# Optimization experiments

Measured on AMD Instinct MI355X. Metric: run time of the kernel, lower is better.

## Reference

```python
import jax, jax.numpy as jnp
import numpy as np

N, E, G = 50000, 400000, 256   # nodes, edges, graphs
DIN, DH = 513, 128             # int(256*4/2+1), dim_h
BN_EPS = 1e-5

def _lin_init(k, fin, fout):
    k1, k2 = jax.random.split(k)
    s = 1.0 / np.sqrt(fin)
    w = jax.random.uniform(k1, (fin, fout), jnp.float32, -s, s)
    b = jax.random.uniform(k2, (fout,), jnp.float32, -s, s)
    return w, b

def setup_inputs():
    ks = list(jax.random.split(jax.random.key(0), 20))
    inp = {
        'x': jax.random.normal(ks[0], (N, DIN), jnp.float32),
        'edge_index': jax.random.randint(ks[1], (2, E), 0, N),
        'batch': jnp.sort(jax.random.randint(ks[2], (N,), 0, G)),
    }
    i = 3
    for c in (1, 2, 3):
        fin = DIN if c == 1 else DH
        w1, b1 = _lin_init(ks[i], fin, DH); i += 1
        w2, b2 = _lin_init(ks[i], DH, DH); i += 1
        inp['conv%d_w1' % c], inp['conv%d_b1' % c] = w1, b1
        inp['conv%d_bn_g' % c] = jnp.ones((DH,), jnp.float32)
        inp['conv%d_bn_b' % c] = jnp.zeros((DH,), jnp.float32)
        inp['conv%d_bn_m' % c] = 0.1 * jax.random.normal(ks[i], (DH,), jnp.float32); i += 1
        inp['conv%d_bn_v' % c] = jax.random.uniform(ks[i], (DH,), jnp.float32, 0.5, 1.5); i += 1
        inp['conv%d_w2' % c], inp['conv%d_b2' % c] = w2, b2
    inp['lin1_w'], inp['lin1_b'] = _lin_init(ks[i], 3 * DH, 3 * DH); i += 1
    inp['lin2_w'], inp['lin2_b'] = _lin_init(ks[i], 3 * DH, 3)
    return inp

def _gin_conv(x, src, dst, w1, b1, g, bb, m, v, w2, b2):
    # GINConv, eps=0: MLP((1+eps)*x + sum_{j->i} x_j)
    agg = jax.ops.segment_sum(x[src], dst, num_segments=x.shape[0])
    h = (x + agg) @ w1 + b1
    h = (h - m) * jax.lax.rsqrt(v + BN_EPS) * g + bb   # BatchNorm1d (eval, running stats)
    h = jax.nn.relu(h)
    return jax.nn.relu(h @ w2 + b2)

def _mean_pool(h, batch, num_graphs):
    s = jax.ops.segment_sum(h, batch, num_segments=num_graphs)
    cnt = jax.ops.segment_sum(jnp.ones((h.shape[0],), h.dtype), batch, num_segments=num_graphs)
    return s / jnp.maximum(cnt, 1.0)[:, None]

def reference(x, edge_index, batch, conv1_w1, conv1_b1, conv1_bn_g, conv1_bn_b, conv1_bn_m, conv1_bn_v, conv1_w2, conv1_b2, conv2_w1, conv2_b1, conv2_bn_g, conv2_bn_b, conv2_bn_m, conv2_bn_v, conv2_w2, conv2_b2, conv3_w1, conv3_b1, conv3_bn_g, conv3_bn_b, conv3_bn_m, conv3_bn_v, conv3_w2, conv3_b2, lin1_w, lin1_b, lin2_w, lin2_b):
    src, dst = edge_index[0], edge_index[1]
    h1 = _gin_conv(x, src, dst, conv1_w1, conv1_b1, conv1_bn_g, conv1_bn_b, conv1_bn_m, conv1_bn_v, conv1_w2, conv1_b2)
    h2 = _gin_conv(h1, src, dst, conv2_w1, conv2_b1, conv2_bn_g, conv2_bn_b, conv2_bn_m, conv2_bn_v, conv2_w2, conv2_b2)
    h3 = _gin_conv(h2, src, dst, conv3_w1, conv3_b1, conv3_bn_g, conv3_bn_b, conv3_bn_m, conv3_bn_v, conv3_w2, conv3_b2)
    h = jnp.concatenate([_mean_pool(h1, batch, G), _mean_pool(h2, batch, G), _mean_pool(h3, batch, G)], axis=1)
    h = jax.nn.relu(h @ lin1_w + lin1_b)   # dropout p=0.5 is identity in eval mode
    return h @ lin2_w + lin2_b
```

## Files before the change

### kernel.cpp

```cpp
#include <hip/hip_runtime.h>

#define NN 50000
#define NE 400000
#define NG 256
#define BN_EPS 1e-5f
#define SCAN_E 8
#define SCAN_CHUNK 2048
#define SCAN_NB 25

typedef __attribute__((ext_vector_type(4))) float f32x4;
typedef __bf16 bf16x8 __attribute__((ext_vector_type(8)));
typedef __bf16 bf16x4 __attribute__((ext_vector_type(4)));

__device__ __forceinline__ void mfma_bf16(f32x4& d, bf16x8 a, bf16x8 b) {
  asm volatile("v_mfma_f32_16x16x32_bf16 %0, %1, %2, %0" : "+v"(d) : "v"(a), "v"(b));
}

__global__ __launch_bounds__(256)
void wprep(const float* __restrict__ W, __bf16* __restrict__ wh,
           __bf16* __restrict__ wl, int K, int Kpad) {
  int idx = blockIdx.x * 256 + threadIdx.x;
  if (idx >= 128 * Kpad) return;
  int n = idx & 127, k = idx >> 7;
  float v = (k < K) ? W[(long)k * 128 + n] : 0.f;
  __bf16 h = (__bf16)v;
  wh[(long)n * Kpad + k] = h;
  wl[(long)n * Kpad + k] = (__bf16)(v - (float)h);
}

template<bool BIAS, bool RELU, bool OUT_SPLIT, bool A_FP32>
__global__ __launch_bounds__(512)
void gemm_bsp(const float* __restrict__ Af,
              const __bf16* __restrict__ Ah, const __bf16* __restrict__ Al,
              const __bf16* __restrict__ Wh, const __bf16* __restrict__ Wl,
              const float* __restrict__ bias, float* __restrict__ Cf,
              __bf16* __restrict__ Ch, __bf16* __restrict__ Cl,
              int M, int Kact, int Kpad) {
  __shared__ __align__(16) __bf16 ah[64 * 40];
  __shared__ __align__(16) __bf16 al[64 * 40];
  __shared__ __align__(16) __bf16 bh[128 * 40];
  __shared__ __align__(16) __bf16 bl[128 * 40];
  const int t = threadIdx.x;
  const int row0 = blockIdx.x * 64;
  const int wave = t >> 6, lane = t & 63;
  const int wr = wave >> 2, wc = wave & 3;
  const int lr = lane & 15, kg = lane >> 4;

  const int b_r = (t >> 2) & 127, b_ko = t & 3;
  const __bf16* bh_src = Wh + (long)b_r * Kpad + b_ko * 8;
  const __bf16* bl_src = Wl + (long)b_r * Kpad + b_ko * 8;
  __bf16* bh_dst = bh + b_r * 40 + b_ko * 8;
  __bf16* bl_dst = bl + b_r * 40 + b_ko * 8;

  f32x4 acc[2][2] = {};
  bf16x8 zero8;
#pragma unroll
  for (int j = 0; j < 8; ++j) zero8[j] = (__bf16)0.f;

  const int a_pl = t >> 8, a_r8 = (t >> 2) & 63, a_ko = t & 3;
  const __bf16* a_src = (a_pl ? Al : Ah) + (long)(row0 + a_r8) * Kpad + a_ko * 8;
  __bf16* a_dst = (a_pl ? al : ah) + a_r8 * 40 + a_ko * 8;
  const bool a_ok8 = (row0 + a_r8) < M;
  const int a_rf = t >> 3, a_kq = t & 7;
  const bool a_okf = (row0 + a_rf) < M;
  const float* af_src = Af + (long)(row0 + a_rf) * Kact + a_kq * 4;
  __bf16* ahf_dst = ah + a_rf * 40 + a_kq * 4;
  __bf16* alf_dst = al + a_rf * 40 + a_kq * 4;

  bf16x8 av;
  float fa[4];
  if (A_FP32) {
#pragma unroll
    for (int j = 0; j < 4; ++j) {
      int k = a_kq * 4 + j;
      fa[j] = (a_okf && k < Kact) ? af_src[j] : 0.f;
    }
  } else {
    av = a_ok8 ? *(const bf16x8*)a_src : zero8;
  }
  bf16x8 bv0 = *(const bf16x8*)bh_src;
  bf16x8 bv1 = *(const bf16x8*)bl_src;

  for (int k0 = 0; k0 < Kpad; k0 += 32) {
    __syncthreads();
    if (A_FP32) {
      bf16x4 hv, lv;
#pragma unroll
      for (int j = 0; j < 4; ++j) {
        __bf16 h = (__bf16)fa[j];
        hv[j] = h; lv[j] = (__bf16)(fa[j] - (float)h);
      }
      *(bf16x4*)ahf_dst = hv;
      *(bf16x4*)alf_dst = lv;
    } else {
      *(bf16x8*)a_dst = av;
    }
    *(bf16x8*)bh_dst = bv0;
    *(bf16x8*)bl_dst = bv1;
    __syncthreads();
    int k1 = k0 + 32;
    if (k1 < Kpad) {
      if (A_FP32) {
#pragma unroll
        for (int j = 0; j < 4; ++j) {
          int k = k1 + a_kq * 4 + j;
          fa[j] = (a_okf && k < Kact) ? af_src[k1 + j] : 0.f;
        }
      } else {
        av = a_ok8 ? *(const bf16x8*)(a_src + k1) : zero8;
      }
      bv0 = *(const bf16x8*)(bh_src + k1);
      bv1 = *(const bf16x8*)(bl_src + k1);
    }
    bf16x8 fah[2], fal[2], fbh[2], fbl[2];
#pragma unroll
    for (int mi = 0; mi < 2; ++mi) {
      int r = wr * 32 + mi * 16 + lr;
      fah[mi] = *(const bf16x8*)&ah[r * 40 + kg * 8];
      fal[mi] = *(const bf16x8*)&al[r * 40 + kg * 8];
    }
#pragma unroll
    for (int ni = 0; ni < 2; ++ni) {
      int c = wc * 32 + ni * 16 + lr;
      fbh[ni] = *(const bf16x8*)&bh[c * 40 + kg * 8];
      fbl[ni] = *(const bf16x8*)&bl[c * 40 + kg * 8];
    }
#pragma unroll
    for (int mi = 0; mi < 2; ++mi)
#pragma unroll
      for (int ni = 0; ni < 2; ++ni) {
        mfma_bf16(acc[mi][ni], fah[mi], fbh[ni]);
        mfma_bf16(acc[mi][ni], fal[mi], fbh[ni]);
        mfma_bf16(acc[mi][ni], fah[mi], fbl[ni]);
      }
  }
#pragma unroll
  for (int mi = 0; mi < 2; ++mi) {
#pragma unroll
    for (int ni = 0; ni < 2; ++ni) {
      int col = wc * 32 + ni * 16 + lr;
      float bv = BIAS ? bias[col] : 0.f;
#pragma unroll
      for (int r = 0; r < 4; ++r) {
        int row = row0 + wr * 32 + mi * 16 + kg * 4 + r;
        if (row < M) {
          float v = acc[mi][ni][r] + bv;
          if (RELU) v = fmaxf(v, 0.f);
          if (OUT_SPLIT) {
            __bf16 h = (__bf16)v;
            Ch[(long)row * 128 + col] = h;
            Cl[(long)row * 128 + col] = (__bf16)(v - (float)h);
          } else {
            Cf[(long)row * 128 + col] = v;
          }
        }
      }
    }
  }
}

__global__ __launch_bounds__(256)
void deg_count(const int* __restrict__ dst, int* __restrict__ deg, int E) {
  int e = blockIdx.x * 256 + threadIdx.x;
  if (e < E) atomicAdd(&deg[dst[e]], 1);
}

__global__ __launch_bounds__(256)
void scan_sums(const int* __restrict__ deg, int* __restrict__ bsum) {
  __shared__ int sm[256];
  int base = blockIdx.x * SCAN_CHUNK + threadIdx.x * SCAN_E;
  int s = 0;
#pragma unroll
  for (int k = 0; k < SCAN_E; ++k) { int i = base + k; if (i < NN) s += deg[i]; }
  sm[threadIdx.x] = s; __syncthreads();
  for (int off = 128; off > 0; off >>= 1) {
    if (threadIdx.x < off) sm[threadIdx.x] += sm[threadIdx.x + off];
    __syncthreads();
  }
  if (threadIdx.x == 0) bsum[blockIdx.x] = sm[0];
}

__global__ void scan_offs(const int* __restrict__ bsum, int* __restrict__ boff,
                          int* __restrict__ rowptr) {
  if (threadIdx.x == 0) {
    int run = 0;
    for (int i = 0; i < SCAN_NB; ++i) { boff[i] = run; run += bsum[i]; }
    rowptr[NN] = run;
  }
}

__global__ __launch_bounds__(256)
void scan_final(const int* __restrict__ boff, int* __restrict__ rowptr,
                int* __restrict__ cursor) {
  __shared__ int sm[256];
  int t = threadIdx.x;
  int base = blockIdx.x * SCAN_CHUNK + t * SCAN_E;
  int v[SCAN_E]; int s = 0;
#pragma unroll
  for (int k = 0; k < SCAN_E; ++k) { int i = base + k; v[k] = (i < NN) ? rowptr[i] : 0; s += v[k]; }
  sm[t] = s; __syncthreads();
  for (int off = 1; off < 256; off <<= 1) {
    int val = sm[t]; int add = (t >= off) ? sm[t - off] : 0;
    __syncthreads();
    sm[t] = val + add;
    __syncthreads();
  }
  int excl = (t == 0 ? 0 : sm[t - 1]) + boff[blockIdx.x];
#pragma unroll
  for (int k = 0; k < SCAN_E; ++k) {
    int i = base + k;
    if (i < NN) { rowptr[i] = excl; cursor[i] = excl; }
    excl += v[k];
  }
}

__global__ __launch_bounds__(256)
void scatter_csr(const int* __restrict__ src, const int* __restrict__ dst,
                 int* __restrict__ cursor, int* __restrict__ csr_src, int E) {
  int e = blockIdx.x * 256 + threadIdx.x;
  if (e < E) {
    int d = dst[e];
    int pos = atomicAdd(&cursor[d], 1);
    csr_src[pos] = src[e];
  }
}

__global__ void bn_prep(const float* __restrict__ b1, const float* __restrict__ g,
                        const float* __restrict__ bb, const float* __restrict__ m,
                        const float* __restrict__ v, float* __restrict__ scale,
                        float* __restrict__ shift) {
  int c = threadIdx.x;
  float s = g[c] * rsqrtf(v[c] + BN_EPS);
  scale[c] = s;
  shift[c] = (b1[c] - m[c]) * s + bb[c];
}

__global__ __launch_bounds__(256)
void gather_bn_split(const float* __restrict__ y, const int* __restrict__ rowptr,
                     const int* __restrict__ csr_src, const float* __restrict__ scale,
                     const float* __restrict__ shift, __bf16* __restrict__ oh,
                     __bf16* __restrict__ ol) {
  const int grp = threadIdx.x >> 5;
  const int lane = threadIdx.x & 31;
  const int node = blockIdx.x * 8 + grp;
  if (node >= NN) return;
  const float4* y4 = (const float4*)y;
  int s = rowptr[node], e = rowptr[node + 1];
  float4 acc = y4[(long)node * 32 + lane];
  float4 acc2 = {0.f, 0.f, 0.f, 0.f};
  int i = s;
  for (; i + 3 < e; i += 4) {
    int s0 = csr_src[i], s1 = csr_src[i + 1], s2 = csr_src[i + 2], s3 = csr_src[i + 3];
    float4 v0 = y4[(long)s0 * 32 + lane];
    float4 v1 = y4[(long)s1 * 32 + lane];
    float4 v2 = y4[(long)s2 * 32 + lane];
    float4 v3 = y4[(long)s3 * 32 + lane];
    acc.x += v0.x; acc.y += v0.y; acc.z += v0.z; acc.w += v0.w;
    acc2.x += v1.x; acc2.y += v1.y; acc2.z += v1.z; acc2.w += v1.w;
    acc.x += v2.x; acc.y += v2.y; acc.z += v2.z; acc.w += v2.w;
    acc2.x += v3.x; acc2.y += v3.y; acc2.z += v3.z; acc2.w += v3.w;
  }
  for (; i < e; ++i) {
    int sn = csr_src[i];
    float4 v = y4[(long)sn * 32 + lane];
    acc.x += v.x; acc.y += v.y; acc.z += v.z; acc.w += v.w;
  }
  acc.x += acc2.x; acc.y += acc2.y; acc.z += acc2.z; acc.w += acc2.w;
  float4 sc = ((const float4*)scale)[lane];
  float4 sh = ((const float4*)shift)[lane];
  float o0 = fmaxf(acc.x * sc.x + sh.x, 0.f);
  float o1 = fmaxf(acc.y * sc.y + sh.y, 0.f);
  float o2 = fmaxf(acc.z * sc.z + sh.z, 0.f);
  float o3 = fmaxf(acc.w * sc.w + sh.w, 0.f);
  __bf16 h0 = (__bf16)o0, h1 = (__bf16)o1, h2 = (__bf16)o2, h3 = (__bf16)o3;
  bf16x4 hv, lv;
  hv[0] = h0; hv[1] = h1; hv[2] = h2; hv[3] = h3;
  lv[0] = (__bf16)(o0 - (float)h0); lv[1] = (__bf16)(o1 - (float)h1);
  lv[2] = (__bf16)(o2 - (float)h2); lv[3] = (__bf16)(o3 - (float)h3);
  *(bf16x4*)&oh[(long)node * 128 + lane * 4] = hv;
  *(bf16x4*)&ol[(long)node * 128 + lane * 4] = lv;
}

__global__ void graph_bounds(const int* __restrict__ batch, int* __restrict__ gstart, int n) {
  int g = blockIdx.x * 64 + threadIdx.x;
  if (g > NG) return;
  int lo = 0, hi = n;
  while (lo < hi) {
    int mid = (lo + hi) >> 1;
    if (batch[mid] < g) lo = mid + 1; else hi = mid;
  }
  gstart[g] = lo;
}

__global__ __launch_bounds__(128)
void pool_mean_split(const __bf16* __restrict__ h0h, const __bf16* __restrict__ h0l,
                     const __bf16* __restrict__ h1h, const __bf16* __restrict__ h1l,
                     const __bf16* __restrict__ h2h, const __bf16* __restrict__ h2l,
                     const int* __restrict__ gstart, float* __restrict__ pooled) {
  int layer = blockIdx.y;
  const __bf16* hh = (layer == 0) ? h0h : (layer == 1) ? h1h : h2h;
  const __bf16* hl = (layer == 0) ? h0l : (layer == 1) ? h1l : h2l;
  int g = blockIdx.x, c = threadIdx.x;
  int s = gstart[g], e = gstart[g + 1];
  float a0 = 0.f, a1 = 0.f, a2 = 0.f, a3 = 0.f;
  int i = s;
  for (; i + 3 < e; i += 4) {
    a0 += (float)hh[(long)i * 128 + c] + (float)hl[(long)i * 128 + c];
    a1 += (float)hh[(long)(i + 1) * 128 + c] + (float)hl[(long)(i + 1) * 128 + c];
    a2 += (float)hh[(long)(i + 2) * 128 + c] + (float)hl[(long)(i + 2) * 128 + c];
    a3 += (float)hh[(long)(i + 3) * 128 + c] + (float)hl[(long)(i + 3) * 128 + c];
  }
  for (; i < e; ++i)
    a0 += (float)hh[(long)i * 128 + c] + (float)hl[(long)i * 128 + c];
  float acc = (a0 + a1) + (a2 + a3);
  pooled[g * 384 + layer * 128 + c] = acc / fmaxf((float)(e - s), 1.f);
}

__global__ __launch_bounds__(384)
void lin1_k(const float* __restrict__ pooled, const float* __restrict__ w,
            const float* __restrict__ b, float* __restrict__ z) {
  __shared__ float pr[384];
  int mrow = blockIdx.x, t = threadIdx.x;
  pr[t] = pooled[mrow * 384 + t];
  __syncthreads();
  float acc = b[t];
  for (int k = 0; k < 384; ++k) acc += pr[k] * w[k * 384 + t];
  z[mrow * 384 + t] = fmaxf(acc, 0.f);
}

__global__ __launch_bounds__(192)
void lin2_k(const float* __restrict__ z, const float* __restrict__ w,
            const float* __restrict__ b, float* __restrict__ out) {
  int idx = blockIdx.x * 192 + threadIdx.x;
  if (idx >= NG * 3) return;
  int mrow = idx / 3, j = idx % 3;
  float acc = b[j];
  for (int k = 0; k < 384; ++k) acc += z[mrow * 384 + k] * w[k * 3 + j];
  out[idx] = acc;
}

extern "C" void kernel_launch(void* const* d_in, const int* in_sizes, int n_in,
                              void* d_out, int out_size, void* d_ws, size_t ws_size,
                              hipStream_t stream) {
  const float* x = (const float*)d_in[0];
  const int* ei = (const int*)d_in[1];
  const int* batch = (const int*)d_in[2];
  const int* srcv = ei;
  const int* dstv = ei + NE;
  const float* cw1[3] = {(const float*)d_in[3], (const float*)d_in[11], (const float*)d_in[19]};
  const float* cb1[3] = {(const float*)d_in[4], (const float*)d_in[12], (const float*)d_in[20]};
  const float* cg[3]  = {(const float*)d_in[5], (const float*)d_in[13], (const float*)d_in[21]};
  const float* cbb[3] = {(const float*)d_in[6], (const float*)d_in[14], (const float*)d_in[22]};
  const float* cm[3]  = {(const float*)d_in[7], (const float*)d_in[15], (const float*)d_in[23]};
  const float* cv[3]  = {(const float*)d_in[8], (const float*)d_in[16], (const float*)d_in[24]};
  const float* cw2[3] = {(const float*)d_in[9], (const float*)d_in[17], (const float*)d_in[25]};
  const float* cb2[3] = {(const float*)d_in[10], (const float*)d_in[18], (const float*)d_in[26]};
  const float* lin1_w = (const float*)d_in[27];
  const float* lin1_b = (const float*)d_in[28];
  const float* lin2_w = (const float*)d_in[29];
  const float* lin2_b = (const float*)d_in[30];

  const size_t NNF = (size_t)NN * 128;
  float* wsf = (float*)d_ws;
  float* y = wsf;
  __bf16* Xb = (__bf16*)(wsf + NNF);
  __bf16* gh = Xb;
  __bf16* gl = Xb + (size_t)6400000;
  __bf16* hh[3], *hl[3];
  for (int c = 0; c < 3; ++c) {
    hh[c] = Xb + (size_t)12800000 + (size_t)c * 12800000;
    hl[c] = hh[c] + (size_t)6400000;
  }
  float* misc = wsf + NNF + (size_t)25600000;
  float* pooled = misc;
  float* z      = pooled + (size_t)NG * 384;
  float* scale  = z + (size_t)NG * 384;
  float* shift  = scale + 128;
  __bf16* wth   = (__bf16*)(shift + 128);
  __bf16* wtl   = wth + (size_t)128 * 544;
  int* rowptr   = (int*)(wtl + (size_t)128 * 544);
  int* cursor   = rowptr + NN + 1;
  int* csr_src  = cursor + NN;
  int* bsum     = csr_src + NE;
  int* boff     = bsum + 32;
  int* gstart   = boff + 64;

  hipMemsetAsync(rowptr, 0, (NN + 1) * sizeof(int), stream);
  deg_count<<<(NE + 255) / 256, 256, 0, stream>>>(dstv, rowptr, NE);
  scan_sums<<<SCAN_NB, 256, 0, stream>>>(rowptr, bsum);
  scan_offs<<<1, 64, 0, stream>>>(bsum, boff, rowptr);
  scan_final<<<SCAN_NB, 256, 0, stream>>>(boff, rowptr, cursor);
  scatter_csr<<<(NE + 255) / 256, 256, 0, stream>>>(srcv, dstv, cursor, csr_src, NE);

  const int gemm_grid = (NN + 63) / 64;
  for (int c = 0; c < 3; ++c) {
    int K = (c == 0) ? 513 : 128;
    int Kpad = (c == 0) ? 544 : 128;
    bn_prep<<<1, 128, 0, stream>>>(cb1[c], cg[c], cbb[c], cm[c], cv[c], scale, shift);
    wprep<<<(128 * Kpad + 255) / 256, 256, 0, stream>>>(cw1[c], wth, wtl, K, Kpad);
    if (c == 0)
      gemm_bsp<false, false, false, true><<<gemm_grid, 512, 0, stream>>>(
          x, nullptr, nullptr, wth, wtl, nullptr, y, nullptr, nullptr, NN, K, Kpad);
    else
      gemm_bsp<false, false, false, false><<<gemm_grid, 512, 0, stream>>>(
          nullptr, hh[c - 1], hl[c - 1], wth, wtl, nullptr, y, nullptr, nullptr, NN, K, Kpad);
    gather_bn_split<<<(NN + 7) / 8, 256, 0, stream>>>(y, rowptr, csr_src, scale, shift, gh, gl);
    wprep<<<(128 * 128 + 255) / 256, 256, 0, stream>>>(cw2[c], wth, wtl, 128, 128);
    gemm_bsp<true, true, true, false><<<gemm_grid, 512, 0, stream>>>(
        nullptr, gh, gl, wth, wtl, cb2[c], nullptr, hh[c], hl[c], NN, 128, 128);
  }
  graph_bounds<<<5, 64, 0, stream>>>(batch, gstart, NN);
  pool_mean_split<<<dim3(NG, 3), 128, 0, stream>>>(hh[0], hl[0], hh[1], hl[1], hh[2], hl[2],
                                                   gstart, pooled);
  lin1_k<<<NG, 384, 0, stream>>>(pooled, lin1_w, lin1_b, z);
  lin2_k<<<4, 192, 0, stream>>>(z, lin2_w, lin2_b, (float*)d_out);
}
```

Measured before the change: 376.8 us.

## Enlarge GEMM tile to 128x128 with 4 waves and widen gather to wave-per-node

The split-bf16 GEMM now uses a 128x128 output tile per 256-thread block. Each wave computes a 64x64 sub-tile (4x4 MFMA fragments), which raises data reuse per LDS load and halves the number of blocks. The fp32-A path now loads 16 contiguous floats per thread, and staging loads are reorganized into 16-element chunks. Separately, the gather/BN kernel maps one 64-lane wave per node with float2 loads instead of 32 lanes with float4. This trades wider vector loads for full-wave occupancy and more in-flight rows, at the cost of more accumulator registers in the GEMM.

After: 423.6 us. +12.4%, slower.

```diff
diff --git a/kernel.cpp b/kernel.cpp
--- a/kernel.cpp
+++ b/kernel.cpp
@@ -11,6 +11,7 @@
 typedef __attribute__((ext_vector_type(4))) float f32x4;
 typedef __bf16 bf16x8 __attribute__((ext_vector_type(8)));
 typedef __bf16 bf16x4 __attribute__((ext_vector_type(4)));
+typedef __bf16 bf16x2 __attribute__((ext_vector_type(2)));
 
 __device__ __forceinline__ void mfma_bf16(f32x4& d, bf16x8 a, bf16x8 b) {
   asm volatile("v_mfma_f32_16x16x32_bf16 %0, %1, %2, %0" : "+v"(d) : "v"(a), "v"(b));
@@ -29,120 +30,128 @@
 }
 
 template<bool BIAS, bool RELU, bool OUT_SPLIT, bool A_FP32>
-__global__ __launch_bounds__(512)
+__global__ __launch_bounds__(256, 3)
 void gemm_bsp(const float* __restrict__ Af,
               const __bf16* __restrict__ Ah, const __bf16* __restrict__ Al,
               const __bf16* __restrict__ Wh, const __bf16* __restrict__ Wl,
               const float* __restrict__ bias, float* __restrict__ Cf,
               __bf16* __restrict__ Ch, __bf16* __restrict__ Cl,
               int M, int Kact, int Kpad) {
-  __shared__ __align__(16) __bf16 ah[64 * 40];
-  __shared__ __align__(16) __bf16 al[64 * 40];
+  __shared__ __align__(16) __bf16 ah[128 * 40];
+  __shared__ __align__(16) __bf16 al[128 * 40];
   __shared__ __align__(16) __bf16 bh[128 * 40];
   __shared__ __align__(16) __bf16 bl[128 * 40];
   const int t = threadIdx.x;
-  const int row0 = blockIdx.x * 64;
+  const int row0 = blockIdx.x * 128;
   const int wave = t >> 6, lane = t & 63;
-  const int wr = wave >> 2, wc = wave & 3;
+  const int wr = wave >> 1, wc = wave & 1;
   const int lr = lane & 15, kg = lane >> 4;
 
-  const int b_r = (t >> 2) & 127, b_ko = t & 3;
-  const __bf16* bh_src = Wh + (long)b_r * Kpad + b_ko * 8;
-  const __bf16* bl_src = Wl + (long)b_r * Kpad + b_ko * 8;
-  __bf16* bh_dst = bh + b_r * 40 + b_ko * 8;
-  __bf16* bl_dst = bl + b_r * 40 + b_ko * 8;
-
-  f32x4 acc[2][2] = {};
+  const int s_r = t >> 1, s_kh = t & 1;
+  const bool a_rok = (row0 + s_r) < M;
+  const __bf16* aph = Ah + (long)(row0 + s_r) * Kpad + s_kh * 16;
+  const __bf16* apl = Al + (long)(row0 + s_r) * Kpad + s_kh * 16;
+  const float*  afp = Af + (long)(row0 + s_r) * Kact + s_kh * 16;
+  const __bf16* bph = Wh + (long)s_r * Kpad + s_kh * 16;
+  const __bf16* bpl = Wl + (long)s_r * Kpad + s_kh * 16;
+  __bf16* a_dh = &ah[s_r * 40 + s_kh * 16];
+  __bf16* a_dl = &al[s_r * 40 + s_kh * 16];
+  __bf16* b_dh = &bh[s_r * 40 + s_kh * 16];
+  __bf16* b_dl = &bl[s_r * 40 + s_kh * 16];
+
+  f32x4 acc[4][4] = {};
   bf16x8 zero8;
 #pragma unroll
   for (int j = 0; j < 8; ++j) zero8[j] = (__bf16)0.f;
 
-  const int a_pl = t >> 8, a_r8 = (t >> 2) & 63, a_ko = t & 3;
-  const __bf16* a_src = (a_pl ? Al : Ah) + (long)(row0 + a_r8) * Kpad + a_ko * 8;
-  __bf16* a_dst = (a_pl ? al : ah) + a_r8 * 40 + a_ko * 8;
-  const bool a_ok8 = (row0 + a_r8) < M;
-  const int a_rf = t >> 3, a_kq = t & 7;
-  const bool a_okf = (row0 + a_rf) < M;
-  const float* af_src = Af + (long)(row0 + a_rf) * Kact + a_kq * 4;
-  __bf16* ahf_dst = ah + a_rf * 40 + a_kq * 4;
-  __bf16* alf_dst = al + a_rf * 40 + a_kq * 4;
-
-  bf16x8 av;
-  float fa[4];
-  if (A_FP32) {
-#pragma unroll
-    for (int j = 0; j < 4; ++j) {
-      int k = a_kq * 4 + j;
-      fa[j] = (a_okf && k < Kact) ? af_src[j] : 0.f;
-    }
-  } else {
-    av = a_ok8 ? *(const bf16x8*)a_src : zero8;
-  }
-  bf16x8 bv0 = *(const bf16x8*)bh_src;
-  bf16x8 bv1 = *(const bf16x8*)bl_src;
+  float fa16[16];
+  bf16x8 rAh0, rAh1, rAl0, rAl1;
+  bf16x8 rBh0, rBh1, rBl0, rBl1;
+
+#define PREFETCH(kb)                                                          \
+  {                                                                           \
+    if (A_FP32) {                                                             \
+      if ((kb) + 32 <= Kact) {                                                \
+        _Pragma("unroll")                                                     \
+        for (int j = 0; j < 16; ++j) fa16[j] = a_rok ? afp[(kb) + j] : 0.f;   \
+      } else {                                                                \
+        _Pragma("unroll")                                                     \
+        for (int j = 0; j < 16; ++j) {                                        \
+          int k = (kb) + s_kh * 16 + j;                                       \
+          fa16[j] = (a_rok && k < Kact) ? afp[(kb) + j] : 0.f;                \
+        }                                                                     \
+      }                                                                       \
+    } else {                                                                  \
+      rAh0 = a_rok ? *(const bf16x8*)(aph + (kb)) : zero8;                    \
+      rAh1 = a_rok ? *(const bf16x8*)(aph + (kb) + 8) : zero8;                \
+      rAl0 = a_rok ? *(const bf16x8*)(apl + (kb)) : zero8;                    \
+      rAl1 = a_rok ? *(const bf16x8*)(apl + (kb) + 8) : zero8;                \
+    }                                                                         \
+    rBh0 = *(const bf16x8*)(bph + (kb));                                      \
+    rBh1 = *(const bf16x8*)(bph + (kb) + 8);                                  \
+    rBl0 = *(const bf16x8*)(bpl + (kb));                                      \
+    rBl1 = *(const bf16x8*)(bpl + (kb) + 8);                                  \
+  }
+
+  PREFETCH(0);
 
   for (int k0 = 0; k0 < Kpad; k0 += 32) {
     __syncthreads();
     if (A_FP32) {
-      bf16x4 hv, lv;
-#pragma unroll
-      for (int j = 0; j < 4; ++j) {
-        __bf16 h = (__bf16)fa[j];
-        hv[j] = h; lv[j] = (__bf16)(fa[j] - (float)h);
+      bf16x8 hv0, hv1, lv0, lv1;
+#pragma unroll
+      for (int j = 0; j < 8; ++j) {
+        __bf16 h = (__bf16)fa16[j];
+        hv0[j] = h; lv0[j] = (__bf16)(fa16[j] - (float)h);
       }
-      *(bf16x4*)ahf_dst = hv;
-      *(bf16x4*)alf_dst = lv;
+#pragma unroll
+      for (int j = 0; j < 8; ++j) {
+        __bf16 h = (__bf16)fa16[8 + j];
+        hv1[j] = h; lv1[j] = (__bf16)(fa16[8 + j] - (float)h);
+      }
+      *(bf16x8*)a_dh = hv0; *(bf16x8*)(a_dh + 8) = hv1;
+      *(bf16x8*)a_dl = lv0; *(bf16x8*)(a_dl + 8) = lv1;
     } else {
-      *(bf16x8*)a_dst = av;
+      *(bf16x8*)a_dh = rAh0; *(bf16x8*)(a_dh + 8) = rAh1;
+      *(bf16x8*)a_dl = rAl0; *(bf16x8*)(a_dl + 8) = rAl1;
     }
-    *(bf16x8*)bh_dst = bv0;
-    *(bf16x8*)bl_dst = bv1;
+    *(bf16x8*)b_dh = rBh0; *(bf16x8*)(b_dh + 8) = rBh1;
+    *(bf16x8*)b_dl = rBl0; *(bf16x8*)(b_dl + 8) = rBl1;
     __syncthreads();
     int k1 = k0 + 32;
-    if (k1 < Kpad) {
-      if (A_FP32) {
-#pragma unroll
-        for (int j = 0; j < 4; ++j) {
-          int k = k1 + a_kq * 4 + j;
-          fa[j] = (a_okf && k < Kact) ? af_src[k1 + j] : 0.f;
-        }
-      } else {
-        av = a_ok8 ? *(const bf16x8*)(a_src + k1) : zero8;
-      }
-      bv0 = *(const bf16x8*)(bh_src + k1);
-      bv1 = *(const bf16x8*)(bl_src + k1);
-    }
-    bf16x8 fah[2], fal[2], fbh[2], fbl[2];
-#pragma unroll
-    for (int mi = 0; mi < 2; ++mi) {
-      int r = wr * 32 + mi * 16 + lr;
+    if (k1 < Kpad) PREFETCH(k1);
+
+    bf16x8 fah[4], fal[4];
+#pragma unroll
+    for (int mi = 0; mi < 4; ++mi) {
+      int r = wr * 64 + mi * 16 + lr;
       fah[mi] = *(const bf16x8*)&ah[r * 40 + kg * 8];
       fal[mi] = *(const bf16x8*)&al[r * 40 + kg * 8];
     }
 #pragma unroll
-    for (int ni = 0; ni < 2; ++ni) {
-      int c = wc * 32 + ni * 16 + lr;
-      fbh[ni] = *(const bf16x8*)&bh[c * 40 + kg * 8];
-      fbl[ni] = *(const bf16x8*)&bl[c * 40 + kg * 8];
+    for (int ni = 0; ni < 4; ++ni) {
+      int c = wc * 64 + ni * 16 + lr;
+      bf16x8 fbh = *(const bf16x8*)&bh[c * 40 + kg * 8];
+      bf16x8 fbl = *(const bf16x8*)&bl[c * 40 + kg * 8];
+#pragma unroll
+      for (int mi = 0; mi < 4; ++mi) mfma_bf16(acc[mi][ni], fah[mi], fbh);
+#pragma unroll
+      for (int mi = 0; mi < 4; ++mi) mfma_bf16(acc[mi][ni], fal[mi], fbh);
+#pragma unroll
+      for (int mi = 0; mi < 4; ++mi) mfma_bf16(acc[mi][ni], fah[mi], fbl);
     }
-#pragma unroll
-    for (int mi = 0; mi < 2; ++mi)
-#pragma unroll
-      for (int ni = 0; ni < 2; ++ni) {
-        mfma_bf16(acc[mi][ni], fah[mi], fbh[ni]);
-        mfma_bf16(acc[mi][ni], fal[mi], fbh[ni]);
-        mfma_bf16(acc[mi][ni], fah[mi], fbl[ni]);
-      }
-  }
-#pragma unroll
-  for (int mi = 0; mi < 2; ++mi) {
-#pragma unroll
-    for (int ni = 0; ni < 2; ++ni) {
-      int col = wc * 32 + ni * 16 + lr;
+  }
+#undef PREFETCH
+
+#pragma unroll
+  for (int mi = 0; mi < 4; ++mi) {
+#pragma unroll
+    for (int ni = 0; ni < 4; ++ni) {
+      int col = wc * 64 + ni * 16 + lr;
       float bv = BIAS ? bias[col] : 0.f;
 #pragma unroll
       for (int r = 0; r < 4; ++r) {
-        int row = row0 + wr * 32 + mi * 16 + kg * 4 + r;
+        int row = row0 + wr * 64 + mi * 16 + kg * 4 + r;
         if (row < M) {
           float v = acc[mi][ni][r] + bv;
           if (RELU) v = fmaxf(v, 0.f);
@@ -240,45 +249,42 @@
                      const int* __restrict__ csr_src, const float* __restrict__ scale,
                      const float* __restrict__ shift, __bf16* __restrict__ oh,
                      __bf16* __restrict__ ol) {
-  const int grp = threadIdx.x >> 5;
-  const int lane = threadIdx.x & 31;
-  const int node = blockIdx.x * 8 + grp;
+  const int wv = threadIdx.x >> 6;
+  const int lane = threadIdx.x & 63;
+  const int node = blockIdx.x * 4 + wv;
   if (node >= NN) return;
-  const float4* y4 = (const float4*)y;
+  const float2* y2 = (const float2*)y;
   int s = rowptr[node], e = rowptr[node + 1];
-  float4 acc = y4[(long)node * 32 + lane];
-  float4 acc2 = {0.f, 0.f, 0.f, 0.f};
+  float2 acc = y2[(long)node * 64 + lane];
+  float2 acc2 = {0.f, 0.f};
   int i = s;
   for (; i + 3 < e; i += 4) {
     int s0 = csr_src[i], s1 = csr_src[i + 1], s2 = csr_src[i + 2], s3 = csr_src[i + 3];
-    float4 v0 = y4[(long)s0 * 32 + lane];
-    float4 v1 = y4[(long)s1 * 32 + lane];
-    float4 v2 = y4[(long)s2 * 32 + lane];
-    float4 v3 = y4[(long)s3 * 32 + lane];
-    acc.x += v0.x; acc.y += v0.y; acc.z += v0.z; acc.w += v0.w;
-    acc2.x += v1.x; acc2.y += v1.y; acc2.z += v1.z; acc2.w += v1.w;
-    acc.x += v2.x; acc.y += v2.y; acc.z += v2.z; acc.w += v2.w;
-    acc2.x += v3.x; acc2.y += v3.y; acc2.z += v3.z; acc2.w += v3.w;
+    float2 v0 = y2[(long)s0 * 64 + lane];
+    float2 v1 = y2[(long)s1 * 64 + lane];
+    float2 v2 = y2[(long)s2 * 64 + lane];
+    float2 v3 = y2[(long)s3 * 64 + lane];
+    acc.x += v0.x; acc.y += v0.y;
+    acc2.x += v1.x; acc2.y += v1.y;
+    acc.x += v2.x; acc.y += v2.y;
+    acc2.x += v3.x; acc2.y += v3.y;
   }
   for (; i < e; ++i) {
     int sn = csr_src[i];
-    float4 v = y4[(long)sn * 32 + lane];
-    acc.x += v.x; acc.y += v.y; acc.z += v.z; acc.w += v.w;
-  }
-  acc.x += acc2.x; acc.y += acc2.y; acc.z += acc2.z; acc.w += acc2.w;
-  float4 sc = ((const float4*)scale)[lane];
-  float4 sh = ((const float4*)shift)[lane];
+    float2 v = y2[(long)sn * 64 + lane];
+    acc.x += v.x; acc.y += v.y;
+  }
+  acc.x += acc2.x; acc.y += acc2.y;
+  float2 sc = ((const float2*)scale)[lane];
+  float2 sh = ((const float2*)shift)[lane];
   float o0 = fmaxf(acc.x * sc.x + sh.x, 0.f);
   float o1 = fmaxf(acc.y * sc.y + sh.y, 0.f);
-  float o2 = fmaxf(acc.z * sc.z + sh.z, 0.f);
-  float o3 = fmaxf(acc.w * sc.w + sh.w, 0.f);
-  __bf16 h0 = (__bf16)o0, h1 = (__bf16)o1, h2 = (__bf16)o2, h3 = (__bf16)o3;
-  bf16x4 hv, lv;
-  hv[0] = h0; hv[1] = h1; hv[2] = h2; hv[3] = h3;
+  __bf16 h0 = (__bf16)o0, h1 = (__bf16)o1;
+  bf16x2 hv, lv;
+  hv[0] = h0; hv[1] = h1;
   lv[0] = (__bf16)(o0 - (float)h0); lv[1] = (__bf16)(o1 - (float)h1);
-  lv[2] = (__bf16)(o2 - (float)h2); lv[3] = (__bf16)(o3 - (float)h3);
-  *(bf16x4*)&oh[(long)node * 128 + lane * 4] = hv;
-  *(bf16x4*)&ol[(long)node * 128 + lane * 4] = lv;
+  *(bf16x2*)&oh[(long)node * 128 + lane * 2] = hv;
+  *(bf16x2*)&ol[(long)node * 128 + lane * 2] = lv;
 }
 
 __global__ void graph_bounds(const int* __restrict__ batch, int* __restrict__ gstart, int n) {
@@ -392,21 +398,21 @@
   scan_final<<<SCAN_NB, 256, 0, stream>>>(boff, rowptr, cursor);
   scatter_csr<<<(NE + 255) / 256, 256, 0, stream>>>(srcv, dstv, cursor, csr_src, NE);
 
-  const int gemm_grid = (NN + 63) / 64;
+  const int gemm_grid = (NN + 127) / 128;
   for (int c = 0; c < 3; ++c) {
     int K = (c == 0) ? 513 : 128;
     int Kpad = (c == 0) ? 544 : 128;
     bn_prep<<<1, 128, 0, stream>>>(cb1[c], cg[c], cbb[c], cm[c], cv[c], scale, shift);
     wprep<<<(128 * Kpad + 255) / 256, 256, 0, stream>>>(cw1[c], wth, wtl, K, Kpad);
     if (c == 0)
-      gemm_bsp<false, false, false, true><<<gemm_grid, 512, 0, stream>>>(
+      gemm_bsp<false, false, false, true><<<gemm_grid, 256, 0, stream>>>(
           x, nullptr, nullptr, wth, wtl, nullptr, y, nullptr, nullptr, NN, K, Kpad);
     else
-      gemm_bsp<false, false, false, false><<<gemm_grid, 512, 0, stream>>>(
+      gemm_bsp<false, false, false, false><<<gemm_grid, 256, 0, stream>>>(
           nullptr, hh[c - 1], hl[c - 1], wth, wtl, nullptr, y, nullptr, nullptr, NN, K, Kpad);
-    gather_bn_split<<<(NN + 7) / 8, 256, 0, stream>>>(y, rowptr, csr_src, scale, shift, gh, gl);
+    gather_bn_split<<<(NN + 3) / 4, 256, 0, stream>>>(y, rowptr, csr_src, scale, shift, gh, gl);
     wprep<<<(128 * 128 + 255) / 256, 256, 0, stream>>>(cw2[c], wth, wtl, 128, 128);
-    gemm_bsp<true, true, true, false><<<gemm_grid, 512, 0, stream>>>(
+    gemm_bsp<true, true, true, false><<<gemm_grid, 256, 0, stream>>>(
         nullptr, gh, gl, wth, wtl, cb2[c], nullptr, hh[c], hl[c], NN, 128, 128);
   }
   graph_bounds<<<5, 64, 0, stream>>>(batch, gstart, NN);
```

## Add register-streamed A GEMM for first-layer 513-wide fp32 input projection

Applied to the files above, without the earlier changes.

Adds a new GEMM kernel used only for the first conv layer. It loads the fp32 A operand straight from global memory into registers, double-buffered in 32-column steps, and splits it to bf16 hi/lo in registers. Only the weight tile is staged in XOR-swizzled shared memory with 64-wide K chunks. Tiles grow to 128 rows per block with 256 threads, and Kpad is raised to 576. The aim is to remove shared-memory staging and barriers for the large activation matrix and to reuse each weight tile across more rows; the cost is higher register pressure and uncoalesced-ish per-lane global reads of A.

After: 388.4 us. 3.1% more time.

```diff
diff --git a/kernel.cpp b/kernel.cpp
--- a/kernel.cpp
+++ b/kernel.cpp
@@ -26,6 +26,136 @@
   __bf16 h = (__bf16)v;
   wh[(long)n * Kpad + k] = h;
   wl[(long)n * Kpad + k] = (__bf16)(v - (float)h);
+}
+
+template<bool BIAS, bool RELU, bool OUT_SPLIT, bool A_FP32>
+__global__ __launch_bounds__(256, 3)
+void gemm_ws(const float* __restrict__ Af,
+             const __bf16* __restrict__ Ah, const __bf16* __restrict__ Al,
+             const __bf16* __restrict__ Wh, const __bf16* __restrict__ Wl,
+             const float* __restrict__ bias, float* __restrict__ Cf,
+             __bf16* __restrict__ Ch, __bf16* __restrict__ Cl,
+             int M, int Kact, int Kpad) {
+  __shared__ __align__(16) __bf16 bsh[128 * 64];
+  __shared__ __align__(16) __bf16 bsl[128 * 64];
+  const int t = threadIdx.x;
+  const int wave = t >> 6, lane = t & 63;
+  const int lr = lane & 15, kg = lane >> 4;
+  const int r0 = blockIdx.x * 128 + wave * 32;
+
+  bool okA[2];
+  const float* apf[2];
+  const __bf16 *aph[2], *apl[2];
+#pragma unroll
+  for (int mi = 0; mi < 2; ++mi) {
+    int row = r0 + mi * 16 + lr;
+    okA[mi] = row < M;
+    long ro = okA[mi] ? (long)row : 0;
+    if (A_FP32) { apf[mi] = Af + ro * Kact + kg * 8; aph[mi] = nullptr; apl[mi] = nullptr; }
+    else { aph[mi] = Ah + ro * Kpad + kg * 8; apl[mi] = Al + ro * Kpad + kg * 8; apf[mi] = nullptr; }
+  }
+
+  f32x4 acc[2][8] = {};
+  bf16x8 zero8;
+#pragma unroll
+  for (int j = 0; j < 8; ++j) zero8[j] = (__bf16)0.f;
+
+  float f0[2][8], f1[2][8];
+  bf16x8 a0h[2], a0l[2], a1h[2], a1l[2];
+
+#define PF(F, AH, AL, KQ)                                                     \
+  if (A_FP32) {                                                               \
+    if ((KQ) + 32 <= Kact) {                                                  \
+      _Pragma("unroll") for (int mi = 0; mi < 2; ++mi)                        \
+      _Pragma("unroll") for (int j = 0; j < 8; ++j)                           \
+        F[mi][j] = okA[mi] ? apf[mi][(KQ) + j] : 0.f;                         \
+    } else {                                                                  \
+      _Pragma("unroll") for (int mi = 0; mi < 2; ++mi)                        \
+      _Pragma("unroll") for (int j = 0; j < 8; ++j) {                         \
+        int k = (KQ) + kg * 8 + j;                                            \
+        F[mi][j] = (okA[mi] && k < Kact) ? apf[mi][(KQ) + j] : 0.f;           \
+      }                                                                       \
+    }                                                                         \
+  } else {                                                                    \
+    _Pragma("unroll") for (int mi = 0; mi < 2; ++mi) {                        \
+      AH[mi] = okA[mi] ? *(const bf16x8*)(aph[mi] + (KQ)) : zero8;            \
+      AL[mi] = okA[mi] ? *(const bf16x8*)(apl[mi] + (KQ)) : zero8;            \
+    }                                                                         \
+  }
+
+#define STEP(F, AH, AL, S)                                                    \
+  {                                                                           \
+    bf16x8 fah[2], fal[2];                                                    \
+    if (A_FP32) {                                                             \
+      _Pragma("unroll") for (int mi = 0; mi < 2; ++mi)                        \
+      _Pragma("unroll") for (int j = 0; j < 8; ++j) {                         \
+        __bf16 h = (__bf16)F[mi][j];                                          \
+        fah[mi][j] = h; fal[mi][j] = (__bf16)(F[mi][j] - (float)h);           \
+      }                                                                       \
+    } else {                                                                  \
+      _Pragma("unroll") for (int mi = 0; mi < 2; ++mi) {                      \
+        fah[mi] = AH[mi]; fal[mi] = AL[mi];                                   \
+      }                                                                       \
+    }                                                                         \
+    _Pragma("unroll") for (int ni = 0; ni < 8; ++ni) {                        \
+      int col = ni * 16 + lr;                                                 \
+      int po = ((S) * 4 + kg) ^ (lr & 7);                                     \
+      bf16x8 fbh = *(const bf16x8*)&bsh[col * 64 + po * 8];                   \
+      bf16x8 fbl = *(const bf16x8*)&bsl[col * 64 + po * 8];                   \
+      _Pragma("unroll") for (int mi = 0; mi < 2; ++mi)                        \
+        mfma_bf16(acc[mi][ni], fah[mi], fbh);                                 \
+      _Pragma("unroll") for (int mi = 0; mi < 2; ++mi)                        \
+        mfma_bf16(acc[mi][ni], fal[mi], fbh);                                 \
+      _Pragma("unroll") for (int mi = 0; mi < 2; ++mi)                        \
+        mfma_bf16(acc[mi][ni], fah[mi], fbl);                                 \
+    }                                                                         \
+  }
+
+  PF(f0, a0h, a0l, 0);
+  for (int kc0 = 0; kc0 < Kpad; kc0 += 64) {
+    __syncthreads();
+#pragma unroll
+    for (int i = 0; i < 4; ++i) {
+      int id = t + i * 256;
+      int col = id >> 3, oct = id & 7;
+      int po = oct ^ (col & 7);
+      *(bf16x8*)&bsh[col * 64 + po * 8] =
+          *(const bf16x8*)&Wh[(long)col * Kpad + kc0 + oct * 8];
+      *(bf16x8*)&bsl[col * 64 + po * 8] =
+          *(const bf16x8*)&Wl[(long)col * Kpad + kc0 + oct * 8];
+    }
+    __syncthreads();
+    PF(f1, a1h, a1l, kc0 + 32);
+    STEP(f0, a0h, a0l, 0);
+    if (kc0 + 64 < Kpad) { PF(f0, a0h, a0l, kc0 + 64); }
+    STEP(f1, a1h, a1l, 1);
+  }
+#undef PF
+#undef STEP
+
+#pragma unroll
+  for (int mi = 0; mi < 2; ++mi) {
+#pragma unroll
+    for (int ni = 0; ni < 8; ++ni) {
+      int col = ni * 16 + lr;
+      float bv = BIAS ? bias[col] : 0.f;
+#pragma unroll
+      for (int r = 0; r < 4; ++r) {
+        int row = r0 + mi * 16 + kg * 4 + r;
+        if (row < M) {
+          float v = acc[mi][ni][r] + bv;
+          if (RELU) v = fmaxf(v, 0.f);
+          if (OUT_SPLIT) {
+            __bf16 h = (__bf16)v;
+            Ch[(long)row * 128 + col] = h;
+            Cl[(long)row * 128 + col] = (__bf16)(v - (float)h);
+          } else {
+            Cf[(long)row * 128 + col] = v;
+          }
+        }
+      }
+    }
+  }
 }
 
 template<bool BIAS, bool RELU, bool OUT_SPLIT, bool A_FP32>
@@ -377,8 +507,8 @@
   float* scale  = z + (size_t)NG * 384;
   float* shift  = scale + 128;
   __bf16* wth   = (__bf16*)(shift + 128);
-  __bf16* wtl   = wth + (size_t)128 * 544;
-  int* rowptr   = (int*)(wtl + (size_t)128 * 544);
+  __bf16* wtl   = wth + (size_t)128 * 576;
+  int* rowptr   = (int*)(wtl + (size_t)128 * 576);
   int* cursor   = rowptr + NN + 1;
   int* csr_src  = cursor + NN;
   int* bsum     = csr_src + NE;
@@ -392,21 +522,22 @@
   scan_final<<<SCAN_NB, 256, 0, stream>>>(boff, rowptr, cursor);
   scatter_csr<<<(NE + 255) / 256, 256, 0, stream>>>(srcv, dstv, cursor, csr_src, NE);
 
-  const int gemm_grid = (NN + 63) / 64;
+  const int ws_grid  = (NN + 127) / 128;
+  const int bsp_grid = (NN + 63) / 64;
   for (int c = 0; c < 3; ++c) {
     int K = (c == 0) ? 513 : 128;
-    int Kpad = (c == 0) ? 544 : 128;
+    int Kpad = (c == 0) ? 576 : 128;
     bn_prep<<<1, 128, 0, stream>>>(cb1[c], cg[c], cbb[c], cm[c], cv[c], scale, shift);
     wprep<<<(128 * Kpad + 255) / 256, 256, 0, stream>>>(cw1[c], wth, wtl, K, Kpad);
     if (c == 0)
-      gemm_bsp<false, false, false, true><<<gemm_grid, 512, 0, stream>>>(
+      gemm_ws<false, false, false, true><<<ws_grid, 256, 0, stream>>>(
           x, nullptr, nullptr, wth, wtl, nullptr, y, nullptr, nullptr, NN, K, Kpad);
     else
-      gemm_bsp<false, false, false, false><<<gemm_grid, 512, 0, stream>>>(
-          nullptr, hh[c - 1], hl[c - 1], wth, wtl, nullptr, y, nullptr, nullptr, NN, K, Kpad);
+      gemm_bsp<false, false, false, false><<<bsp_grid, 512, 0, stream>>>(
+          nullptr, hh[c - 1], hl[c - 1], wth, wtl, nullptr, y, nullptr, nullptr, NN, 128, 128);
     gather_bn_split<<<(NN + 7) / 8, 256, 0, stream>>>(y, rowptr, csr_src, scale, shift, gh, gl);
     wprep<<<(128 * 128 + 255) / 256, 256, 0, stream>>>(cw2[c], wth, wtl, 128, 128);
-    gemm_bsp<true, true, true, false><<<gemm_grid, 512, 0, stream>>>(
+    gemm_bsp<true, true, true, false><<<bsp_grid, 512, 0, stream>>>(
         nullptr, gh, gl, wth, wtl, cb2[c], nullptr, hh[c], hl[c], NN, 128, 128);
   }
   graph_bounds<<<5, 64, 0, stream>>>(batch, gstart, NN);
```
